# Kernel tuning notes

Measured on AMD Instinct MI355X. Metric: run time of the kernel, lower is better.

Reference implementation:

```python
import jax, jax.numpy as jnp
import numpy as np

N_NODES = 16384
N_EDGES = 262144
D = 256
B = 32            # graphs per batch; nodes_per_graph = N_NODES // B
N_LAYERS = 3
N_HIDDEN = 2


def setup_inputs() -> dict:
    key = jax.random.key(0)
    ks = jax.random.split(key, 10)
    s = 1.0 / np.sqrt(D)
    x = jax.random.normal(ks[0], (N_NODES, D), dtype=jnp.float32)
    edge_index = jax.random.randint(ks[1], (2, N_EDGES), 0, N_NODES, dtype=jnp.int64)
    # SAGEConv params: lin_l (applied to aggregated neighbors, has bias), lin_r (root, no bias)
    Wl = jax.random.uniform(ks[2], (N_LAYERS, D, D), jnp.float32, -s, s)
    bl = jax.random.uniform(ks[3], (N_LAYERS, D), jnp.float32, -s, s)
    Wr = jax.random.uniform(ks[4], (N_LAYERS, D, D), jnp.float32, -s, s)
    # post MLP: two relu hidden layers + linear output (rlkit Mlp defaults)
    Wh = jax.random.uniform(ks[5], (N_HIDDEN, D, D), jnp.float32, -s, s)
    bh = jax.random.uniform(ks[6], (N_HIDDEN, D), jnp.float32, -s, s)
    Wo = jax.random.uniform(ks[7], (D, D), jnp.float32, -s, s)
    bo = jax.random.uniform(ks[8], (D,), jnp.float32, -s, s)
    return {"x": x, "edge_index": edge_index, "Wl": Wl, "bl": bl, "Wr": Wr,
            "Wh": Wh, "bh": bh, "Wo": Wo, "bo": bo}


def reference(x, edge_index, Wl, bl, Wr, Wh, bh, Wo, bo):
    src, dst = edge_index[0], edge_index[1]
    # in-degree for mean aggregation (computed once; edge structure is fixed)
    deg = jax.ops.segment_sum(jnp.ones((src.shape[0],), x.dtype), dst,
                              num_segments=N_NODES)
    inv_deg = (1.0 / jnp.maximum(deg, 1.0))[:, None]          # [N,1]
    for l in range(N_LAYERS):
        # gather -> segment mean -> dual GEMM (SAGEConv, aggr='mean')
        agg = jax.ops.segment_sum(x[src], dst, num_segments=N_NODES) * inv_deg
        x = agg @ Wl[l] + bl[l] + x @ Wr[l]                   # [N,D]
    h = x.reshape(B, -1, D)[:, 0, :]                          # root node per graph [B,D]
    for l in range(N_HIDDEN):
        h = jax.nn.relu(h @ Wh[l] + bh[l])
    return h @ Wo + bo                                        # [B,D]
```

## Files before the change

### kernel.cpp

```cpp
#include <hip/hip_runtime.h>

#define N_NODES 16384
#define N_EDGES 262144
#define D 256
#define B_GRAPHS 32
#define NODES_PER_GRAPH 512
#define MAXDEG 64

__global__ __launch_bounds__(256) void zero_cnt_kernel(int* __restrict__ cnt) {
    cnt[blockIdx.x * 256 + threadIdx.x] = 0;
}

__global__ __launch_bounds__(256) void fill_bucket_kernel(const int* __restrict__ edge,
                                                          int* __restrict__ cnt,
                                                          int* __restrict__ col) {
    int e = blockIdx.x * 256 + threadIdx.x;
    int dst = edge[N_EDGES + e];
    int src = edge[e];
    int slot = atomicAdd(&cnt[dst], 1);
    if (slot < MAXDEG) col[dst * MAXDEG + slot] = src;
}

__global__ __launch_bounds__(256) void aggx_kernel(const float* __restrict__ x,
                                                   const int* __restrict__ cnt,
                                                   const int* __restrict__ col,
                                                   float* __restrict__ A) {
    int node = blockIdx.x * 4 + (threadIdx.x >> 6);
    int lane = threadIdx.x & 63;
    int c = cnt[node];
    if (c > MAXDEG) c = MAXDEG;
    int my = (lane < c) ? col[node * MAXDEG + lane] : 0;
    float a0 = 0.f, a1 = 0.f, a2 = 0.f, a3 = 0.f;
    int j = 0;
    for (; j + 8 <= c; j += 8) {
        float4 v[8];
        #pragma unroll
        for (int q = 0; q < 8; ++q) {
            int s = __shfl(my, j + q);
            v[q] = *(const float4*)&x[(size_t)s * D + lane * 4];
        }
        #pragma unroll
        for (int q = 0; q < 8; ++q) {
            a0 += v[q].x; a1 += v[q].y; a2 += v[q].z; a3 += v[q].w;
        }
    }
    for (; j < c; ++j) {
        int s = __shfl(my, j);
        float4 v = *(const float4*)&x[(size_t)s * D + lane * 4];
        a0 += v.x; a1 += v.y; a2 += v.z; a3 += v.w;
    }
    float id = 1.0f / (float)(c < 1 ? 1 : c);
    float4 r = make_float4(a0 * id, a1 * id, a2 * id, a3 * id);
    *(float4*)&A[(size_t)node * D + lane * 4] = r;
}

__global__ __launch_bounds__(1024) void tail_kernel(
    const int* __restrict__ cnt, const int* __restrict__ col,
    const float* __restrict__ x, const float* __restrict__ A,
    const float* __restrict__ Wl, const float* __restrict__ bl,
    const float* __restrict__ Wr,
    const float* __restrict__ Wh, const float* __restrict__ bh,
    const float* __restrict__ Wo, const float* __restrict__ bo,
    float* __restrict__ out)
{
    __shared__ float g0[D], g1[D], g2[D], g3[D];
    __shared__ float v0[D], v1[D], v2[D], hA[D], hB[D];
    __shared__ float part1[16][D];
    __shared__ float part2[16][D];
    __shared__ int nbr[MAXDEG];
    __shared__ int snr;

    const int b = blockIdx.x, t = threadIdx.x;
    const int w = t >> 6, lane = t & 63;
    const int root = b * NODES_PER_GRAPH;

    if (t == 0) { int cc = cnt[root]; snr = (cc > MAXDEG) ? MAXDEG : cc; }
    __syncthreads();
    const int c0 = snr;
    if (t < c0) nbr[t] = col[root * MAXDEG + t];
    if (t < D) {
        g0[t] = x[(size_t)root * D + t];
        g1[t] = A[(size_t)root * D + t];
    }
    __syncthreads();

    float p1[4] = {0.f, 0.f, 0.f, 0.f}, p2[4] = {0.f, 0.f, 0.f, 0.f};
    for (int i = w; i < c0; i += 16) {
        int n = nbr[i];
        {
            float4 v = *(const float4*)&A[(size_t)n * D + lane * 4];
            p1[0] += v.x; p1[1] += v.y; p1[2] += v.z; p1[3] += v.w;
        }
        int c = cnt[n]; if (c > MAXDEG) c = MAXDEG;
        int my = (lane < c) ? col[n * MAXDEG + lane] : 0;
        float a[4] = {0.f, 0.f, 0.f, 0.f};
        int j = 0;
        for (; j + 4 <= c; j += 4) {
            float4 v[4];
            #pragma unroll
            for (int q = 0; q < 4; ++q) {
                int s = __shfl(my, j + q);
                v[q] = *(const float4*)&A[(size_t)s * D + lane * 4];
            }
            #pragma unroll
            for (int q = 0; q < 4; ++q) {
                a[0] += v[q].x; a[1] += v[q].y; a[2] += v[q].z; a[3] += v[q].w;
            }
        }
        for (; j < c; ++j) {
            int s = __shfl(my, j);
            float4 v = *(const float4*)&A[(size_t)s * D + lane * 4];
            a[0] += v.x; a[1] += v.y; a[2] += v.z; a[3] += v.w;
        }
        float id = 1.0f / (float)(c < 1 ? 1 : c);
        #pragma unroll
        for (int q = 0; q < 4; ++q) p2[q] += a[q] * id;
    }
    #pragma unroll
    for (int q = 0; q < 4; ++q) {
        part1[w][lane * 4 + q] = p1[q];
        part2[w][lane * 4 + q] = p2[q];
    }
    __syncthreads();
    if (t < D) {
        float s1 = 0.f, s2 = 0.f;
        #pragma unroll
        for (int ww = 0; ww < 16; ++ww) { s1 += part1[ww][t]; s2 += part2[ww][t]; }
        float id0 = 1.0f / (float)(c0 < 1 ? 1 : c0);
        g2[t] = s1 * id0;
        g3[t] = s2 * id0;
    }
    __syncthreads();

    const int c = t & 255, kq = t >> 8;
    {
        const float* WL = Wl;
        const float* WR = Wr;
        float a0 = 0.f, a1 = 0.f, a2 = 0.f;
        #pragma unroll 8
        for (int k0 = 0; k0 < 64; ++k0) {
            int k = kq * 64 + k0;
            float wl = WL[(size_t)k * D + c];
            float wr = WR[(size_t)k * D + c];
            a0 += g1[k] * wl + g0[k] * wr;
            a1 += g2[k] * wl + g1[k] * wr;
            a2 += g3[k] * wl + g2[k] * wr;
        }
        part1[kq][c] = a0; part1[4 + kq][c] = a1; part1[8 + kq][c] = a2;
        __syncthreads();
        if (t < D) {
            float bb = bl[t];
            v0[t] = part1[0][t] + part1[1][t] + part1[2][t] + part1[3][t] + bb;
            v1[t] = part1[4][t] + part1[5][t] + part1[6][t] + part1[7][t] + bb;
            v2[t] = part1[8][t] + part1[9][t] + part1[10][t] + part1[11][t] + bb;
        }
        __syncthreads();
    }
    {
        const float* WL = Wl + (size_t)1 * D * D;
        const float* WR = Wr + (size_t)1 * D * D;
        float aA = 0.f, aB = 0.f;
        #pragma unroll 8
        for (int k0 = 0; k0 < 64; ++k0) {
            int k = kq * 64 + k0;
            float wl = WL[(size_t)k * D + c];
            float wr = WR[(size_t)k * D + c];
            aA += v2[k] * wl + v1[k] * wr;
            aB += v1[k] * wl + v0[k] * wr;
        }
        part1[kq][c] = aA; part1[4 + kq][c] = aB;
        __syncthreads();
        if (t < D) {
            float bb = bl[D + t];
            hA[t] = part1[0][t] + part1[1][t] + part1[2][t] + part1[3][t] + bb;
            hB[t] = part1[4][t] + part1[5][t] + part1[6][t] + part1[7][t] + bb;
        }
        __syncthreads();
    }
    {
        const float* WL = Wl + (size_t)2 * D * D;
        const float* WR = Wr + (size_t)2 * D * D;
        float acc = 0.f;
        #pragma unroll 8
        for (int k0 = 0; k0 < 64; ++k0) {
            int k = kq * 64 + k0;
            acc += hA[k] * WL[(size_t)k * D + c] + hB[k] * WR[(size_t)k * D + c];
        }
        part1[kq][c] = acc;
        __syncthreads();
        if (t < D) v0[t] = part1[0][t] + part1[1][t] + part1[2][t] + part1[3][t]
                           + bl[2 * D + t];
        __syncthreads();
    }
    for (int l = 0; l < 3; ++l) {
        const float* W = (l < 2) ? Wh + (size_t)l * D * D : Wo;
        float acc = 0.f;
        #pragma unroll 8
        for (int k0 = 0; k0 < 64; ++k0) {
            int k = kq * 64 + k0;
            acc += v0[k] * W[(size_t)k * D + c];
        }
        part1[kq][c] = acc;
        __syncthreads();
        if (t < D) {
            float v = part1[0][t] + part1[1][t] + part1[2][t] + part1[3][t]
                    + ((l < 2) ? bh[(size_t)l * D + t] : bo[t]);
            if (l < 2) v0[t] = fmaxf(v, 0.f);
            else       out[(size_t)b * D + t] = v;
        }
        __syncthreads();
    }
}

extern "C" void kernel_launch(void* const* d_in, const int* in_sizes, int n_in,
                              void* d_out, int out_size, void* d_ws, size_t ws_size,
                              hipStream_t stream) {
    const float* x    = (const float*)d_in[0];
    const int*   edge = (const int*)d_in[1];
    const float* Wl   = (const float*)d_in[2];
    const float* bl   = (const float*)d_in[3];
    const float* Wr   = (const float*)d_in[4];
    const float* Wh   = (const float*)d_in[5];
    const float* bh   = (const float*)d_in[6];
    const float* Wo   = (const float*)d_in[7];
    const float* bo   = (const float*)d_in[8];
    float* out = (float*)d_out;

    char* w = (char*)d_ws;
    auto alloc = [&](size_t bytes) {
        char* p = w;
        w += (bytes + 255) & ~(size_t)255;
        return p;
    };
    int*   cnt = (int*)  alloc((size_t)N_NODES * 4);
    int*   col = (int*)  alloc((size_t)N_NODES * MAXDEG * 4);
    float* A   = (float*)alloc((size_t)N_NODES * D * 4);

    zero_cnt_kernel<<<N_NODES / 256, 256, 0, stream>>>(cnt);
    fill_bucket_kernel<<<N_EDGES / 256, 256, 0, stream>>>(edge, cnt, col);
    aggx_kernel<<<N_NODES / 4, 256, 0, stream>>>(x, cnt, col, A);
    tail_kernel<<<B_GRAPHS, 1024, 0, stream>>>(cnt, col, x, A,
                                               Wl, bl, Wr, Wh, bh, Wo, bo, out);
}
```

Baseline: 94.94 us.

## Split root 2-hop neighbor aggregation into separate wide kernel, vectorize tail GEMVs

The second-hop neighbor aggregation for each graph's root now runs in a new kernel with one wavefront per (graph, neighbor slot), 2048 wavefronts in total. Before, it ran inside the 32-block tail kernel, so only 32 blocks did that work. The tail kernel now just sums the precomputed rows. Its GEMV loops also switch to float4 weight loads with 16 k-partitions instead of 4. The cost is one extra launch and a small workspace buffer.

```diff
diff --git a/kernel.cpp b/kernel.cpp
--- a/kernel.cpp
+++ b/kernel.cpp
@@ -54,9 +54,48 @@
     *(float4*)&A[(size_t)node * D + lane * 4] = r;
 }
 
+__global__ __launch_bounds__(256) void aggB_kernel(const float* __restrict__ A,
+                                                   const int* __restrict__ cnt,
+                                                   const int* __restrict__ col,
+                                                   float* __restrict__ B) {
+    int wg = blockIdx.x * 4 + (threadIdx.x >> 6);
+    int r = wg >> 6;
+    int slot = wg & 63;
+    int lane = threadIdx.x & 63;
+    int root = r * NODES_PER_GRAPH;
+    int c0 = cnt[root]; if (c0 > MAXDEG) c0 = MAXDEG;
+    if (slot >= c0) return;
+    int n = col[root * MAXDEG + slot];
+    int c = cnt[n]; if (c > MAXDEG) c = MAXDEG;
+    int my = (lane < c) ? col[n * MAXDEG + lane] : 0;
+    float a0 = 0.f, a1 = 0.f, a2 = 0.f, a3 = 0.f;
+    int j = 0;
+    for (; j + 8 <= c; j += 8) {
+        float4 v[8];
+        #pragma unroll
+        for (int q = 0; q < 8; ++q) {
+            int s = __shfl(my, j + q);
+            v[q] = *(const float4*)&A[(size_t)s * D + lane * 4];
+        }
+        #pragma unroll
+        for (int q = 0; q < 8; ++q) {
+            a0 += v[q].x; a1 += v[q].y; a2 += v[q].z; a3 += v[q].w;
+        }
+    }
+    for (; j < c; ++j) {
+        int s = __shfl(my, j);
+        float4 v = *(const float4*)&A[(size_t)s * D + lane * 4];
+        a0 += v.x; a1 += v.y; a2 += v.z; a3 += v.w;
+    }
+    float id = 1.0f / (float)(c < 1 ? 1 : c);
+    float4 out = make_float4(a0 * id, a1 * id, a2 * id, a3 * id);
+    *(float4*)&B[(size_t)wg * D + lane * 4] = out;
+}
+
 __global__ __launch_bounds__(1024) void tail_kernel(
     const int* __restrict__ cnt, const int* __restrict__ col,
     const float* __restrict__ x, const float* __restrict__ A,
+    const float* __restrict__ B,
     const float* __restrict__ Wl, const float* __restrict__ bl,
     const float* __restrict__ Wr,
     const float* __restrict__ Wh, const float* __restrict__ bh,
@@ -65,9 +104,7 @@
 {
     __shared__ float g0[D], g1[D], g2[D], g3[D];
     __shared__ float v0[D], v1[D], v2[D], hA[D], hB[D];
-    __shared__ float part1[16][D];
-    __shared__ float part2[16][D];
-    __shared__ int nbr[MAXDEG];
+    __shared__ float part[3][16][D];
     __shared__ int snr;
 
     const int b = blockIdx.x, t = threadIdx.x;
@@ -75,136 +112,139 @@
     const int root = b * NODES_PER_GRAPH;
 
     if (t == 0) { int cc = cnt[root]; snr = (cc > MAXDEG) ? MAXDEG : cc; }
-    __syncthreads();
-    const int c0 = snr;
-    if (t < c0) nbr[t] = col[root * MAXDEG + t];
     if (t < D) {
         g0[t] = x[(size_t)root * D + t];
         g1[t] = A[(size_t)root * D + t];
     }
     __syncthreads();
-
-    float p1[4] = {0.f, 0.f, 0.f, 0.f}, p2[4] = {0.f, 0.f, 0.f, 0.f};
-    for (int i = w; i < c0; i += 16) {
-        int n = nbr[i];
-        {
-            float4 v = *(const float4*)&A[(size_t)n * D + lane * 4];
-            p1[0] += v.x; p1[1] += v.y; p1[2] += v.z; p1[3] += v.w;
-        }
-        int c = cnt[n]; if (c > MAXDEG) c = MAXDEG;
-        int my = (lane < c) ? col[n * MAXDEG + lane] : 0;
-        float a[4] = {0.f, 0.f, 0.f, 0.f};
-        int j = 0;
-        for (; j + 4 <= c; j += 4) {
-            float4 v[4];
-            #pragma unroll
-            for (int q = 0; q < 4; ++q) {
-                int s = __shfl(my, j + q);
-                v[q] = *(const float4*)&A[(size_t)s * D + lane * 4];
+    const int c0 = snr;
+
+    {
+        float p1[4] = {0.f, 0.f, 0.f, 0.f}, p2[4] = {0.f, 0.f, 0.f, 0.f};
+        for (int i = w; i < c0; i += 16) {
+            int n = col[root * MAXDEG + i];
+            float4 va = *(const float4*)&A[(size_t)n * D + lane * 4];
+            float4 vb = *(const float4*)&B[(size_t)(b * MAXDEG + i) * D + lane * 4];
+            p1[0] += va.x; p1[1] += va.y; p1[2] += va.z; p1[3] += va.w;
+            p2[0] += vb.x; p2[1] += vb.y; p2[2] += vb.z; p2[3] += vb.w;
+        }
+        #pragma unroll
+        for (int q = 0; q < 4; ++q) {
+            part[0][w][lane * 4 + q] = p1[q];
+            part[1][w][lane * 4 + q] = p2[q];
+        }
+        __syncthreads();
+        if (t < D) {
+            float s1 = 0.f, s2 = 0.f;
+            #pragma unroll
+            for (int ww = 0; ww < 16; ++ww) { s1 += part[0][ww][t]; s2 += part[1][ww][t]; }
+            float id0 = 1.0f / (float)(c0 < 1 ? 1 : c0);
+            g2[t] = s1 * id0;
+            g3[t] = s2 * id0;
+        }
+        __syncthreads();
+    }
+
+    const int kq = t >> 6, c4 = t & 63;
+    {
+        const float4* WL = (const float4*)Wl;
+        const float4* WR = (const float4*)Wr;
+        float4 a0 = {0,0,0,0}, a1 = {0,0,0,0}, a2 = {0,0,0,0};
+        #pragma unroll
+        for (int k0 = 0; k0 < 16; ++k0) {
+            int k = kq * 16 + k0;
+            float4 wl = WL[(size_t)k * 64 + c4];
+            float4 wr = WR[(size_t)k * 64 + c4];
+            float h1 = g1[k], h0 = g0[k], h2 = g2[k], h3 = g3[k];
+            a0.x += h1 * wl.x + h0 * wr.x; a0.y += h1 * wl.y + h0 * wr.y;
+            a0.z += h1 * wl.z + h0 * wr.z; a0.w += h1 * wl.w + h0 * wr.w;
+            a1.x += h2 * wl.x + h1 * wr.x; a1.y += h2 * wl.y + h1 * wr.y;
+            a1.z += h2 * wl.z + h1 * wr.z; a1.w += h2 * wl.w + h1 * wr.w;
+            a2.x += h3 * wl.x + h2 * wr.x; a2.y += h3 * wl.y + h2 * wr.y;
+            a2.z += h3 * wl.z + h2 * wr.z; a2.w += h3 * wl.w + h2 * wr.w;
+        }
+        *(float4*)&part[0][kq][c4 * 4] = a0;
+        *(float4*)&part[1][kq][c4 * 4] = a1;
+        *(float4*)&part[2][kq][c4 * 4] = a2;
+        __syncthreads();
+        if (t < D) {
+            float s0 = 0.f, s1 = 0.f, s2 = 0.f;
+            #pragma unroll
+            for (int i = 0; i < 16; ++i) {
+                s0 += part[0][i][t]; s1 += part[1][i][t]; s2 += part[2][i][t];
             }
-            #pragma unroll
-            for (int q = 0; q < 4; ++q) {
-                a[0] += v[q].x; a[1] += v[q].y; a[2] += v[q].z; a[3] += v[q].w;
-            }
-        }
-        for (; j < c; ++j) {
-            int s = __shfl(my, j);
-            float4 v = *(const float4*)&A[(size_t)s * D + lane * 4];
-            a[0] += v.x; a[1] += v.y; a[2] += v.z; a[3] += v.w;
-        }
-        float id = 1.0f / (float)(c < 1 ? 1 : c);
-        #pragma unroll
-        for (int q = 0; q < 4; ++q) p2[q] += a[q] * id;
-    }
-    #pragma unroll
-    for (int q = 0; q < 4; ++q) {
-        part1[w][lane * 4 + q] = p1[q];
-        part2[w][lane * 4 + q] = p2[q];
-    }
-    __syncthreads();
-    if (t < D) {
-        float s1 = 0.f, s2 = 0.f;
-        #pragma unroll
-        for (int ww = 0; ww < 16; ++ww) { s1 += part1[ww][t]; s2 += part2[ww][t]; }
-        float id0 = 1.0f / (float)(c0 < 1 ? 1 : c0);
-        g2[t] = s1 * id0;
-        g3[t] = s2 * id0;
-    }
-    __syncthreads();
-
-    const int c = t & 255, kq = t >> 8;
-    {
-        const float* WL = Wl;
-        const float* WR = Wr;
-        float a0 = 0.f, a1 = 0.f, a2 = 0.f;
-        #pragma unroll 8
-        for (int k0 = 0; k0 < 64; ++k0) {
-            int k = kq * 64 + k0;
-            float wl = WL[(size_t)k * D + c];
-            float wr = WR[(size_t)k * D + c];
-            a0 += g1[k] * wl + g0[k] * wr;
-            a1 += g2[k] * wl + g1[k] * wr;
-            a2 += g3[k] * wl + g2[k] * wr;
-        }
-        part1[kq][c] = a0; part1[4 + kq][c] = a1; part1[8 + kq][c] = a2;
-        __syncthreads();
-        if (t < D) {
             float bb = bl[t];
-            v0[t] = part1[0][t] + part1[1][t] + part1[2][t] + part1[3][t] + bb;
-            v1[t] = part1[4][t] + part1[5][t] + part1[6][t] + part1[7][t] + bb;
-            v2[t] = part1[8][t] + part1[9][t] + part1[10][t] + part1[11][t] + bb;
-        }
-        __syncthreads();
-    }
-    {
-        const float* WL = Wl + (size_t)1 * D * D;
-        const float* WR = Wr + (size_t)1 * D * D;
-        float aA = 0.f, aB = 0.f;
-        #pragma unroll 8
-        for (int k0 = 0; k0 < 64; ++k0) {
-            int k = kq * 64 + k0;
-            float wl = WL[(size_t)k * D + c];
-            float wr = WR[(size_t)k * D + c];
-            aA += v2[k] * wl + v1[k] * wr;
-            aB += v1[k] * wl + v0[k] * wr;
-        }
-        part1[kq][c] = aA; part1[4 + kq][c] = aB;
-        __syncthreads();
-        if (t < D) {
+            v0[t] = s0 + bb; v1[t] = s1 + bb; v2[t] = s2 + bb;
+        }
+        __syncthreads();
+    }
+    {
+        const float4* WL = (const float4*)(Wl + (size_t)1 * D * D);
+        const float4* WR = (const float4*)(Wr + (size_t)1 * D * D);
+        float4 aA = {0,0,0,0}, aB = {0,0,0,0};
+        #pragma unroll
+        for (int k0 = 0; k0 < 16; ++k0) {
+            int k = kq * 16 + k0;
+            float4 wl = WL[(size_t)k * 64 + c4];
+            float4 wr = WR[(size_t)k * 64 + c4];
+            float h2 = v2[k], h1 = v1[k], h0 = v0[k];
+            aA.x += h2 * wl.x + h1 * wr.x; aA.y += h2 * wl.y + h1 * wr.y;
+            aA.z += h2 * wl.z + h1 * wr.z; aA.w += h2 * wl.w + h1 * wr.w;
+            aB.x += h1 * wl.x + h0 * wr.x; aB.y += h1 * wl.y + h0 * wr.y;
+            aB.z += h1 * wl.z + h0 * wr.z; aB.w += h1 * wl.w + h0 * wr.w;
+        }
+        *(float4*)&part[0][kq][c4 * 4] = aA;
+        *(float4*)&part[1][kq][c4 * 4] = aB;
+        __syncthreads();
+        if (t < D) {
+            float sA = 0.f, sB = 0.f;
+            #pragma unroll
+            for (int i = 0; i < 16; ++i) { sA += part[0][i][t]; sB += part[1][i][t]; }
             float bb = bl[D + t];
-            hA[t] = part1[0][t] + part1[1][t] + part1[2][t] + part1[3][t] + bb;
-            hB[t] = part1[4][t] + part1[5][t] + part1[6][t] + part1[7][t] + bb;
-        }
-        __syncthreads();
-    }
-    {
-        const float* WL = Wl + (size_t)2 * D * D;
-        const float* WR = Wr + (size_t)2 * D * D;
-        float acc = 0.f;
-        #pragma unroll 8
-        for (int k0 = 0; k0 < 64; ++k0) {
-            int k = kq * 64 + k0;
-            acc += hA[k] * WL[(size_t)k * D + c] + hB[k] * WR[(size_t)k * D + c];
-        }
-        part1[kq][c] = acc;
-        __syncthreads();
-        if (t < D) v0[t] = part1[0][t] + part1[1][t] + part1[2][t] + part1[3][t]
-                           + bl[2 * D + t];
+            hA[t] = sA + bb; hB[t] = sB + bb;
+        }
+        __syncthreads();
+    }
+    {
+        const float4* WL = (const float4*)(Wl + (size_t)2 * D * D);
+        const float4* WR = (const float4*)(Wr + (size_t)2 * D * D);
+        float4 a = {0,0,0,0};
+        #pragma unroll
+        for (int k0 = 0; k0 < 16; ++k0) {
+            int k = kq * 16 + k0;
+            float4 wl = WL[(size_t)k * 64 + c4];
+            float4 wr = WR[(size_t)k * 64 + c4];
+            float ha = hA[k], hb = hB[k];
+            a.x += ha * wl.x + hb * wr.x; a.y += ha * wl.y + hb * wr.y;
+            a.z += ha * wl.z + hb * wr.z; a.w += ha * wl.w + hb * wr.w;
+        }
+        *(float4*)&part[0][kq][c4 * 4] = a;
+        __syncthreads();
+        if (t < D) {
+            float s = 0.f;
+            #pragma unroll
+            for (int i = 0; i < 16; ++i) s += part[0][i][t];
+            v0[t] = s + bl[2 * D + t];
+        }
         __syncthreads();
     }
     for (int l = 0; l < 3; ++l) {
-        const float* W = (l < 2) ? Wh + (size_t)l * D * D : Wo;
-        float acc = 0.f;
-        #pragma unroll 8
-        for (int k0 = 0; k0 < 64; ++k0) {
-            int k = kq * 64 + k0;
-            acc += v0[k] * W[(size_t)k * D + c];
-        }
-        part1[kq][c] = acc;
-        __syncthreads();
-        if (t < D) {
-            float v = part1[0][t] + part1[1][t] + part1[2][t] + part1[3][t]
-                    + ((l < 2) ? bh[(size_t)l * D + t] : bo[t]);
+        const float4* W = (const float4*)((l < 2) ? Wh + (size_t)l * D * D : Wo);
+        float4 a = {0,0,0,0};
+        #pragma unroll
+        for (int k0 = 0; k0 < 16; ++k0) {
+            int k = kq * 16 + k0;
+            float4 wv = W[(size_t)k * 64 + c4];
+            float hk = v0[k];
+            a.x += hk * wv.x; a.y += hk * wv.y; a.z += hk * wv.z; a.w += hk * wv.w;
+        }
+        *(float4*)&part[0][kq][c4 * 4] = a;
+        __syncthreads();
+        if (t < D) {
+            float s = 0.f;
+            #pragma unroll
+            for (int i = 0; i < 16; ++i) s += part[0][i][t];
+            float v = s + ((l < 2) ? bh[(size_t)l * D + t] : bo[t]);
             if (l < 2) v0[t] = fmaxf(v, 0.f);
             else       out[(size_t)b * D + t] = v;
         }
@@ -235,10 +275,12 @@
     int*   cnt = (int*)  alloc((size_t)N_NODES * 4);
     int*   col = (int*)  alloc((size_t)N_NODES * MAXDEG * 4);
     float* A   = (float*)alloc((size_t)N_NODES * D * 4);
+    float* B   = (float*)alloc((size_t)B_GRAPHS * MAXDEG * D * 4);
 
     zero_cnt_kernel<<<N_NODES / 256, 256, 0, stream>>>(cnt);
     fill_bucket_kernel<<<N_EDGES / 256, 256, 0, stream>>>(edge, cnt, col);
     aggx_kernel<<<N_NODES / 4, 256, 0, stream>>>(x, cnt, col, A);
-    tail_kernel<<<B_GRAPHS, 1024, 0, stream>>>(cnt, col, x, A,
+    aggB_kernel<<<512, 256, 0, stream>>>(A, cnt, col, B);
+    tail_kernel<<<B_GRAPHS, 1024, 0, stream>>>(cnt, col, x, A, B,
                                                Wl, bl, Wr, Wh, bh, Wo, bo, out);
 }
```

New measurement: 113.0 us, median of 2. 19.0% more time.

## Prefetch weights into L2 during aggregation and batch weight loads in tail

Applied to the files above, without the earlier changes.

Adds 36 extra blocks to the aggregation kernel that read all Wl, Wr, Wh and Wo weights into cache, so the single-wave tail kernel finds them warm in L2 instead of fetching them cold from HBM. The tail kernel's GEMV loops now load 16 or 32 weight values into registers before the FMAs, giving more loads in flight. The neighbor-of-neighbor gather unroll goes from 4 to 8. The cost is extra register pressure in the 1024-thread tail kernel and a small amount of wasted bandwidth during aggregation.

```diff
diff --git a/kernel.cpp b/kernel.cpp
--- a/kernel.cpp
+++ b/kernel.cpp
@@ -6,6 +6,7 @@
 #define B_GRAPHS 32
 #define NODES_PER_GRAPH 512
 #define MAXDEG 64
+#define NWARM 36
 
 __global__ __launch_bounds__(256) void zero_cnt_kernel(int* __restrict__ cnt) {
     cnt[blockIdx.x * 256 + threadIdx.x] = 0;
@@ -24,9 +25,33 @@
 __global__ __launch_bounds__(256) void aggx_kernel(const float* __restrict__ x,
                                                    const int* __restrict__ cnt,
                                                    const int* __restrict__ col,
-                                                   float* __restrict__ A) {
-    int node = blockIdx.x * 4 + (threadIdx.x >> 6);
-    int lane = threadIdx.x & 63;
+                                                   float* __restrict__ A,
+                                                   const float* __restrict__ Wl,
+                                                   const float* __restrict__ Wr,
+                                                   const float* __restrict__ Wh,
+                                                   const float* __restrict__ Wo,
+                                                   float* __restrict__ warm) {
+    const int bid = blockIdx.x;
+    const int t = threadIdx.x;
+    if (bid >= 4096) {
+        int wb = bid - 4096;
+        float s = 0.f;
+        #pragma unroll
+        for (int i = 0; i < 16; ++i) {
+            size_t fidx = ((size_t)wb * 4096 + i * 256 + t) * 4;
+            const float* src; size_t off = fidx;
+            if (off < 196608)      { src = Wl; }
+            else if (off < 393216) { src = Wr; off -= 196608; }
+            else if (off < 524288) { src = Wh; off -= 393216; }
+            else                   { src = Wo; off -= 524288; }
+            float4 v = *(const float4*)&src[off];
+            s += v.x + v.y + v.z + v.w;
+        }
+        warm[wb * 256 + t] = s;
+        return;
+    }
+    int node = bid * 4 + (t >> 6);
+    int lane = t & 63;
     int c = cnt[node];
     if (c > MAXDEG) c = MAXDEG;
     int my = (lane < c) ? col[node * MAXDEG + lane] : 0;
@@ -84,75 +109,88 @@
     }
     __syncthreads();
 
-    float p1[4] = {0.f, 0.f, 0.f, 0.f}, p2[4] = {0.f, 0.f, 0.f, 0.f};
-    for (int i = w; i < c0; i += 16) {
-        int n = nbr[i];
-        {
-            float4 v = *(const float4*)&A[(size_t)n * D + lane * 4];
-            p1[0] += v.x; p1[1] += v.y; p1[2] += v.z; p1[3] += v.w;
-        }
-        int c = cnt[n]; if (c > MAXDEG) c = MAXDEG;
-        int my = (lane < c) ? col[n * MAXDEG + lane] : 0;
-        float a[4] = {0.f, 0.f, 0.f, 0.f};
-        int j = 0;
-        for (; j + 4 <= c; j += 4) {
-            float4 v[4];
-            #pragma unroll
-            for (int q = 0; q < 4; ++q) {
-                int s = __shfl(my, j + q);
-                v[q] = *(const float4*)&A[(size_t)s * D + lane * 4];
-            }
-            #pragma unroll
-            for (int q = 0; q < 4; ++q) {
-                a[0] += v[q].x; a[1] += v[q].y; a[2] += v[q].z; a[3] += v[q].w;
-            }
-        }
-        for (; j < c; ++j) {
-            int s = __shfl(my, j);
-            float4 v = *(const float4*)&A[(size_t)s * D + lane * 4];
-            a[0] += v.x; a[1] += v.y; a[2] += v.z; a[3] += v.w;
-        }
-        float id = 1.0f / (float)(c < 1 ? 1 : c);
+    {
+        float p1[4] = {0.f, 0.f, 0.f, 0.f}, p2[4] = {0.f, 0.f, 0.f, 0.f};
+        for (int i = w; i < c0; i += 16) {
+            int n = nbr[i];
+            {
+                float4 v = *(const float4*)&A[(size_t)n * D + lane * 4];
+                p1[0] += v.x; p1[1] += v.y; p1[2] += v.z; p1[3] += v.w;
+            }
+            int c = cnt[n]; if (c > MAXDEG) c = MAXDEG;
+            int my = (lane < c) ? col[n * MAXDEG + lane] : 0;
+            float a[4] = {0.f, 0.f, 0.f, 0.f};
+            int j = 0;
+            for (; j + 8 <= c; j += 8) {
+                float4 v[8];
+                #pragma unroll
+                for (int q = 0; q < 8; ++q) {
+                    int s = __shfl(my, j + q);
+                    v[q] = *(const float4*)&A[(size_t)s * D + lane * 4];
+                }
+                #pragma unroll
+                for (int q = 0; q < 8; ++q) {
+                    a[0] += v[q].x; a[1] += v[q].y; a[2] += v[q].z; a[3] += v[q].w;
+                }
+            }
+            for (; j < c; ++j) {
+                int s = __shfl(my, j);
+                float4 v = *(const float4*)&A[(size_t)s * D + lane * 4];
+                a[0] += v.x; a[1] += v.y; a[2] += v.z; a[3] += v.w;
+            }
+            float id = 1.0f / (float)(c < 1 ? 1 : c);
+            #pragma unroll
+            for (int q = 0; q < 4; ++q) p2[q] += a[q] * id;
+        }
         #pragma unroll
-        for (int q = 0; q < 4; ++q) p2[q] += a[q] * id;
-    }
-    #pragma unroll
-    for (int q = 0; q < 4; ++q) {
-        part1[w][lane * 4 + q] = p1[q];
-        part2[w][lane * 4 + q] = p2[q];
-    }
-    __syncthreads();
-    if (t < D) {
-        float s1 = 0.f, s2 = 0.f;
-        #pragma unroll
-        for (int ww = 0; ww < 16; ++ww) { s1 += part1[ww][t]; s2 += part2[ww][t]; }
-        float id0 = 1.0f / (float)(c0 < 1 ? 1 : c0);
-        g2[t] = s1 * id0;
-        g3[t] = s2 * id0;
-    }
-    __syncthreads();
+        for (int q = 0; q < 4; ++q) {
+            part1[w][lane * 4 + q] = p1[q];
+            part2[w][lane * 4 + q] = p2[q];
+        }
+        __syncthreads();
+        if (t < D) {
+            float s1 = 0.f, s2 = 0.f;
+            #pragma unroll
+            for (int ww = 0; ww < 16; ++ww) { s1 += part1[ww][t]; s2 += part2[ww][t]; }
+            float id0 = 1.0f / (float)(c0 < 1 ? 1 : c0);
+            g2[t] = s1 * id0;
+            g3[t] = s2 * id0;
+        }
+        __syncthreads();
+    }
 
     const int c = t & 255, kq = t >> 8;
     {
         const float* WL = Wl;
         const float* WR = Wr;
         float a0 = 0.f, a1 = 0.f, a2 = 0.f;
-        #pragma unroll 8
-        for (int k0 = 0; k0 < 64; ++k0) {
-            int k = kq * 64 + k0;
-            float wl = WL[(size_t)k * D + c];
-            float wr = WR[(size_t)k * D + c];
-            a0 += g1[k] * wl + g0[k] * wr;
-            a1 += g2[k] * wl + g1[k] * wr;
-            a2 += g3[k] * wl + g2[k] * wr;
+        for (int kb = 0; kb < 64; kb += 16) {
+            float wl[16], wr[16];
+            #pragma unroll
+            for (int q = 0; q < 16; ++q) {
+                int k = kq * 64 + kb + q;
+                wl[q] = WL[(size_t)k * D + c];
+                wr[q] = WR[(size_t)k * D + c];
+            }
+            #pragma unroll
+            for (int q = 0; q < 16; ++q) {
+                int k = kq * 64 + kb + q;
+                float h0 = g0[k], h1 = g1[k], h2 = g2[k], h3 = g3[k];
+                a0 += h1 * wl[q] + h0 * wr[q];
+                a1 += h2 * wl[q] + h1 * wr[q];
+                a2 += h3 * wl[q] + h2 * wr[q];
+            }
         }
         part1[kq][c] = a0; part1[4 + kq][c] = a1; part1[8 + kq][c] = a2;
         __syncthreads();
         if (t < D) {
+            float s0 = 0.f, s1 = 0.f, s2 = 0.f;
+            #pragma unroll
+            for (int i = 0; i < 4; ++i) {
+                s0 += part1[i][t]; s1 += part1[4 + i][t]; s2 += part1[8 + i][t];
+            }
             float bb = bl[t];
-            v0[t] = part1[0][t] + part1[1][t] + part1[2][t] + part1[3][t] + bb;
-            v1[t] = part1[4][t] + part1[5][t] + part1[6][t] + part1[7][t] + bb;
-            v2[t] = part1[8][t] + part1[9][t] + part1[10][t] + part1[11][t] + bb;
+            v0[t] = s0 + bb; v1[t] = s1 + bb; v2[t] = s2 + bb;
         }
         __syncthreads();
     }
@@ -160,51 +198,80 @@
         const float* WL = Wl + (size_t)1 * D * D;
         const float* WR = Wr + (size_t)1 * D * D;
         float aA = 0.f, aB = 0.f;
-        #pragma unroll 8
-        for (int k0 = 0; k0 < 64; ++k0) {
-            int k = kq * 64 + k0;
-            float wl = WL[(size_t)k * D + c];
-            float wr = WR[(size_t)k * D + c];
-            aA += v2[k] * wl + v1[k] * wr;
-            aB += v1[k] * wl + v0[k] * wr;
+        for (int kb = 0; kb < 64; kb += 16) {
+            float wl[16], wr[16];
+            #pragma unroll
+            for (int q = 0; q < 16; ++q) {
+                int k = kq * 64 + kb + q;
+                wl[q] = WL[(size_t)k * D + c];
+                wr[q] = WR[(size_t)k * D + c];
+            }
+            #pragma unroll
+            for (int q = 0; q < 16; ++q) {
+                int k = kq * 64 + kb + q;
+                float h2 = v2[k], h1 = v1[k], h0 = v0[k];
+                aA += h2 * wl[q] + h1 * wr[q];
+                aB += h1 * wl[q] + h0 * wr[q];
+            }
         }
         part1[kq][c] = aA; part1[4 + kq][c] = aB;
         __syncthreads();
         if (t < D) {
+            float sA = 0.f, sB = 0.f;
+            #pragma unroll
+            for (int i = 0; i < 4; ++i) { sA += part1[i][t]; sB += part1[4 + i][t]; }
             float bb = bl[D + t];
-            hA[t] = part1[0][t] + part1[1][t] + part1[2][t] + part1[3][t] + bb;
-            hB[t] = part1[4][t] + part1[5][t] + part1[6][t] + part1[7][t] + bb;
+            hA[t] = sA + bb; hB[t] = sB + bb;
         }
         __syncthreads();
     }
     {
         const float* WL = Wl + (size_t)2 * D * D;
         const float* WR = Wr + (size_t)2 * D * D;
-        float acc = 0.f;
-        #pragma unroll 8
-        for (int k0 = 0; k0 < 64; ++k0) {
-            int k = kq * 64 + k0;
-            acc += hA[k] * WL[(size_t)k * D + c] + hB[k] * WR[(size_t)k * D + c];
-        }
-        part1[kq][c] = acc;
-        __syncthreads();
-        if (t < D) v0[t] = part1[0][t] + part1[1][t] + part1[2][t] + part1[3][t]
-                           + bl[2 * D + t];
+        float a = 0.f;
+        for (int kb = 0; kb < 64; kb += 16) {
+            float wl[16], wr[16];
+            #pragma unroll
+            for (int q = 0; q < 16; ++q) {
+                int k = kq * 64 + kb + q;
+                wl[q] = WL[(size_t)k * D + c];
+                wr[q] = WR[(size_t)k * D + c];
+            }
+            #pragma unroll
+            for (int q = 0; q < 16; ++q) {
+                int k = kq * 64 + kb + q;
+                a += hA[k] * wl[q] + hB[k] * wr[q];
+            }
+        }
+        part1[kq][c] = a;
+        __syncthreads();
+        if (t < D) {
+            float s = 0.f;
+            #pragma unroll
+            for (int i = 0; i < 4; ++i) s += part1[i][t];
+            v0[t] = s + bl[2 * D + t];
+        }
         __syncthreads();
     }
     for (int l = 0; l < 3; ++l) {
         const float* W = (l < 2) ? Wh + (size_t)l * D * D : Wo;
-        float acc = 0.f;
-        #pragma unroll 8
-        for (int k0 = 0; k0 < 64; ++k0) {
-            int k = kq * 64 + k0;
-            acc += v0[k] * W[(size_t)k * D + c];
-        }
-        part1[kq][c] = acc;
-        __syncthreads();
-        if (t < D) {
-            float v = part1[0][t] + part1[1][t] + part1[2][t] + part1[3][t]
-                    + ((l < 2) ? bh[(size_t)l * D + t] : bo[t]);
+        float a = 0.f;
+        for (int kb = 0; kb < 64; kb += 32) {
+            float wv[32];
+            #pragma unroll
+            for (int q = 0; q < 32; ++q)
+                wv[q] = W[(size_t)(kq * 64 + kb + q) * D + c];
+            #pragma unroll
+            for (int q = 0; q < 32; ++q)
+                a += v0[kq * 64 + kb + q] * wv[q];
+        }
+        part1[kq][c] = a;
+        __syncthreads();
+        if (t < D) {
+            float s = 0.f;
+            #pragma unroll
+            for (int i = 0; i < 4; ++i) s += part1[i][t];
+            float v = s + ((l < 2) ? bh[(size_t)l * D + t] : bo[t]);
             if (l < 2) v0[t] = fmaxf(v, 0.f);
             else       out[(size_t)b * D + t] = v;
         }
@@ -232,13 +299,15 @@
         w += (bytes + 255) & ~(size_t)255;
         return p;
     };
-    int*   cnt = (int*)  alloc((size_t)N_NODES * 4);
-    int*   col = (int*)  alloc((size_t)N_NODES * MAXDEG * 4);
-    float* A   = (float*)alloc((size_t)N_NODES * D * 4);
+    int*   cnt  = (int*)  alloc((size_t)N_NODES * 4);
+    int*   col  = (int*)  alloc((size_t)N_NODES * MAXDEG * 4);
+    float* A    = (float*)alloc((size_t)N_NODES * D * 4);
+    float* warm = (float*)alloc((size_t)NWARM * 256 * 4);
 
     zero_cnt_kernel<<<N_NODES / 256, 256, 0, stream>>>(cnt);
     fill_bucket_kernel<<<N_EDGES / 256, 256, 0, stream>>>(edge, cnt, col);
-    aggx_kernel<<<N_NODES / 4, 256, 0, stream>>>(x, cnt, col, A);
+    aggx_kernel<<<4096 + NWARM, 256, 0, stream>>>(x, cnt, col, A,
+                                                  Wl, Wr, Wh, Wo, warm);
     tail_kernel<<<B_GRAPHS, 1024, 0, stream>>>(cnt, col, x, A,
                                                Wl, bl, Wr, Wh, bh, Wo, bo, out);
 }
```

Result: slower. 133.4 us (+40.5%).

## Precompose SAGE layer weight products into Q matrices computed alongside edge/aggregation kernels

Applied to the files above, without the earlier changes.

Because the SAGE layers are linear, the three layers' Wl/Wr matrices are pre-multiplied into four composite 256x256 matrices Q (plus an effective bias), so the tail needs one four-term matvec instead of three dependent layered GEMV stages. The weight products run as extra blocks inside the edge-bucketing and aggregation kernels, overlapping the scatter/gather work. This trades serial per-graph tail work for redundant dense GEMM work per call and changes floating-point association. The tail's neighbor gather is also unrolled by eight, and the MLP loads are batched.

```diff
diff --git a/kernel.cpp b/kernel.cpp
--- a/kernel.cpp
+++ b/kernel.cpp
@@ -11,60 +11,179 @@
     cnt[blockIdx.x * 256 + threadIdx.x] = 0;
 }
 
-__global__ __launch_bounds__(256) void fill_bucket_kernel(const int* __restrict__ edge,
-                                                          int* __restrict__ cnt,
-                                                          int* __restrict__ col) {
-    int e = blockIdx.x * 256 + threadIdx.x;
-    int dst = edge[N_EDGES + e];
-    int src = edge[e];
-    int slot = atomicAdd(&cnt[dst], 1);
-    if (slot < MAXDEG) col[dst * MAXDEG + slot] = src;
-}
-
-__global__ __launch_bounds__(256) void aggx_kernel(const float* __restrict__ x,
-                                                   const int* __restrict__ cnt,
-                                                   const int* __restrict__ col,
-                                                   float* __restrict__ A) {
-    int node = blockIdx.x * 4 + (threadIdx.x >> 6);
-    int lane = threadIdx.x & 63;
-    int c = cnt[node];
-    if (c > MAXDEG) c = MAXDEG;
-    int my = (lane < c) ? col[node * MAXDEG + lane] : 0;
-    float a0 = 0.f, a1 = 0.f, a2 = 0.f, a3 = 0.f;
-    int j = 0;
-    for (; j + 8 <= c; j += 8) {
-        float4 v[8];
-        #pragma unroll
-        for (int q = 0; q < 8; ++q) {
-            int s = __shfl(my, j + q);
-            v[q] = *(const float4*)&x[(size_t)s * D + lane * 4];
-        }
-        #pragma unroll
-        for (int q = 0; q < 8; ++q) {
-            a0 += v[q].x; a1 += v[q].y; a2 += v[q].z; a3 += v[q].w;
-        }
-    }
-    for (; j < c; ++j) {
-        int s = __shfl(my, j);
-        float4 v = *(const float4*)&x[(size_t)s * D + lane * 4];
-        a0 += v.x; a1 += v.y; a2 += v.z; a3 += v.w;
-    }
-    float id = 1.0f / (float)(c < 1 ? 1 : c);
-    float4 r = make_float4(a0 * id, a1 * id, a2 * id, a3 * id);
-    *(float4*)&A[(size_t)node * D + lane * 4] = r;
+__device__ __forceinline__ void mm_tile32(const float* __restrict__ A,
+                                          const float* __restrict__ B,
+                                          int r0, int c0,
+                                          float (*As)[257], float acc[4]) {
+    const int t = threadIdx.x;
+    __syncthreads();
+    #pragma unroll
+    for (int i = 0; i < 8; ++i) {
+        int idx = i * 256 + t;
+        int r = idx >> 6, cq = idx & 63;
+        float4 v = *(const float4*)&A[(size_t)(r0 + r) * D + cq * 4];
+        As[r][cq * 4 + 0] = v.x; As[r][cq * 4 + 1] = v.y;
+        As[r][cq * 4 + 2] = v.z; As[r][cq * 4 + 3] = v.w;
+    }
+    __syncthreads();
+    const int c = c0 + (t & 31);
+    const int rb = t >> 5;
+    #pragma unroll 8
+    for (int k = 0; k < 256; ++k) {
+        float bv = B[(size_t)k * D + c];
+        acc[0] += As[rb][k] * bv;
+        acc[1] += As[rb + 8][k] * bv;
+        acc[2] += As[rb + 16][k] * bv;
+        acc[3] += As[rb + 24][k] * bv;
+    }
+}
+
+__device__ __forceinline__ void mm_store(float* __restrict__ O, int r0, int c0,
+                                         const float acc[4]) {
+    const int t = threadIdx.x;
+    const int c = c0 + (t & 31);
+    const int rb = t >> 5;
+    #pragma unroll
+    for (int q = 0; q < 4; ++q)
+        O[(size_t)(r0 + rb + q * 8) * D + c] = acc[q];
+}
+
+__global__ __launch_bounds__(256) void fill_p_kernel(
+    const int* __restrict__ edge, int* __restrict__ cnt, int* __restrict__ col,
+    const float* __restrict__ Wl, const float* __restrict__ Wr,
+    const float* __restrict__ bl,
+    float* __restrict__ P2, float* __restrict__ P1, float* __restrict__ P0,
+    float* __restrict__ bias2)
+{
+    __shared__ float As[32][257];
+    const int bid = blockIdx.x;
+    const int t = threadIdx.x;
+    if (bid < 1024) {
+        int e = bid * 256 + t;
+        int dst = edge[N_EDGES + e];
+        int src = edge[e];
+        int slot = atomicAdd(&cnt[dst], 1);
+        if (slot < MAXDEG) col[dst * MAXDEG + slot] = src;
+        return;
+    }
+    if (bid == 1216) {
+        const float* b2 = bl + D;
+        const float* b3 = bl + 2 * D;
+        const float* L3 = Wl + (size_t)2 * D * D;
+        const float* R3 = Wr + (size_t)2 * D * D;
+        float s = 0.f;
+        #pragma unroll 8
+        for (int k = 0; k < D; ++k)
+            s += b2[k] * (L3[(size_t)k * D + t] + R3[(size_t)k * D + t]);
+        bias2[t] = s + b3[t];
+        return;
+    }
+    int pb = bid - 1024;
+    int mat = pb >> 6, tile = pb & 63;
+    int r0 = (tile >> 3) * 32, c0 = (tile & 7) * 32;
+    const float* L2 = Wl + (size_t)1 * D * D;
+    const float* R2 = Wr + (size_t)1 * D * D;
+    const float* L3 = Wl + (size_t)2 * D * D;
+    const float* R3 = Wr + (size_t)2 * D * D;
+    float acc[4] = {0.f, 0.f, 0.f, 0.f};
+    if (mat == 0) {
+        mm_tile32(L2, L3, r0, c0, As, acc);
+        mm_store(P2, r0, c0, acc);
+    } else if (mat == 1) {
+        mm_tile32(R2, L3, r0, c0, As, acc);
+        mm_tile32(L2, R3, r0, c0, As, acc);
+        mm_store(P1, r0, c0, acc);
+    } else {
+        mm_tile32(R2, R3, r0, c0, As, acc);
+        mm_store(P0, r0, c0, acc);
+    }
+}
+
+__global__ __launch_bounds__(256) void aggx_q_kernel(
+    const float* __restrict__ x, const int* __restrict__ cnt,
+    const int* __restrict__ col, float* __restrict__ A,
+    const float* __restrict__ Wl, const float* __restrict__ Wr,
+    const float* __restrict__ bl,
+    const float* __restrict__ P2, const float* __restrict__ P1,
+    const float* __restrict__ P0, const float* __restrict__ bias2,
+    float* __restrict__ Q, float* __restrict__ beff)
+{
+    __shared__ float As[32][257];
+    const int bid = blockIdx.x;
+    const int t = threadIdx.x;
+    if (bid < 4096) {
+        int node = bid * 4 + (t >> 6);
+        int lane = t & 63;
+        int c = cnt[node];
+        if (c > MAXDEG) c = MAXDEG;
+        int my = (lane < c) ? col[node * MAXDEG + lane] : 0;
+        float a0 = 0.f, a1 = 0.f, a2 = 0.f, a3 = 0.f;
+        int j = 0;
+        for (; j + 8 <= c; j += 8) {
+            float4 v[8];
+            #pragma unroll
+            for (int q = 0; q < 8; ++q) {
+                int s = __shfl(my, j + q);
+                v[q] = *(const float4*)&x[(size_t)s * D + lane * 4];
+            }
+            #pragma unroll
+            for (int q = 0; q < 8; ++q) {
+                a0 += v[q].x; a1 += v[q].y; a2 += v[q].z; a3 += v[q].w;
+            }
+        }
+        for (; j < c; ++j) {
+            int s = __shfl(my, j);
+            float4 v = *(const float4*)&x[(size_t)s * D + lane * 4];
+            a0 += v.x; a1 += v.y; a2 += v.z; a3 += v.w;
+        }
+        float id = 1.0f / (float)(c < 1 ? 1 : c);
+        float4 r = make_float4(a0 * id, a1 * id, a2 * id, a3 * id);
+        *(float4*)&A[(size_t)node * D + lane * 4] = r;
+        return;
+    }
+    if (bid == 4352) {
+        const float* b1 = bl;
+        float s = 0.f;
+        #pragma unroll 8
+        for (int k = 0; k < D; ++k)
+            s += b1[k] * (P2[(size_t)k * D + t] + P1[(size_t)k * D + t]
+                        + P0[(size_t)k * D + t]);
+        beff[t] = s + bias2[t];
+        return;
+    }
+    int qb = bid - 4096;
+    int mat = qb >> 6, tile = qb & 63;
+    int r0 = (tile >> 3) * 32, c0 = (tile & 7) * 32;
+    const float* L1 = Wl;
+    const float* R1 = Wr;
+    float acc[4] = {0.f, 0.f, 0.f, 0.f};
+    if (mat == 0) {
+        mm_tile32(L1, P2, r0, c0, As, acc);
+        mm_store(Q + 3 * (size_t)D * D, r0, c0, acc);
+    } else if (mat == 1) {
+        mm_tile32(R1, P2, r0, c0, As, acc);
+        mm_tile32(L1, P1, r0, c0, As, acc);
+        mm_store(Q + 2 * (size_t)D * D, r0, c0, acc);
+    } else if (mat == 2) {
+        mm_tile32(R1, P1, r0, c0, As, acc);
+        mm_tile32(L1, P0, r0, c0, As, acc);
+        mm_store(Q + 1 * (size_t)D * D, r0, c0, acc);
+    } else {
+        mm_tile32(R1, P0, r0, c0, As, acc);
+        mm_store(Q + 0 * (size_t)D * D, r0, c0, acc);
+    }
 }
 
 __global__ __launch_bounds__(1024) void tail_kernel(
     const int* __restrict__ cnt, const int* __restrict__ col,
     const float* __restrict__ x, const float* __restrict__ A,
-    const float* __restrict__ Wl, const float* __restrict__ bl,
-    const float* __restrict__ Wr,
+    const float* __restrict__ Q, const float* __restrict__ beff,
     const float* __restrict__ Wh, const float* __restrict__ bh,
     const float* __restrict__ Wo, const float* __restrict__ bo,
     float* __restrict__ out)
 {
     __shared__ float g0[D], g1[D], g2[D], g3[D];
-    __shared__ float v0[D], v1[D], v2[D], hA[D], hB[D];
+    __shared__ float v0[D];
     __shared__ float part1[16][D];
     __shared__ float part2[16][D];
     __shared__ int nbr[MAXDEG];
@@ -84,123 +203,91 @@
     }
     __syncthreads();
 
-    float p1[4] = {0.f, 0.f, 0.f, 0.f}, p2[4] = {0.f, 0.f, 0.f, 0.f};
-    for (int i = w; i < c0; i += 16) {
-        int n = nbr[i];
-        {
-            float4 v = *(const float4*)&A[(size_t)n * D + lane * 4];
-            p1[0] += v.x; p1[1] += v.y; p1[2] += v.z; p1[3] += v.w;
-        }
-        int c = cnt[n]; if (c > MAXDEG) c = MAXDEG;
-        int my = (lane < c) ? col[n * MAXDEG + lane] : 0;
-        float a[4] = {0.f, 0.f, 0.f, 0.f};
-        int j = 0;
-        for (; j + 4 <= c; j += 4) {
-            float4 v[4];
-            #pragma unroll
-            for (int q = 0; q < 4; ++q) {
-                int s = __shfl(my, j + q);
-                v[q] = *(const float4*)&A[(size_t)s * D + lane * 4];
-            }
-            #pragma unroll
-            for (int q = 0; q < 4; ++q) {
-                a[0] += v[q].x; a[1] += v[q].y; a[2] += v[q].z; a[3] += v[q].w;
-            }
-        }
-        for (; j < c; ++j) {
-            int s = __shfl(my, j);
-            float4 v = *(const float4*)&A[(size_t)s * D + lane * 4];
-            a[0] += v.x; a[1] += v.y; a[2] += v.z; a[3] += v.w;
-        }
-        float id = 1.0f / (float)(c < 1 ? 1 : c);
+    {
+        float p1[4] = {0.f, 0.f, 0.f, 0.f}, p2[4] = {0.f, 0.f, 0.f, 0.f};
+        for (int i = w; i < c0; i += 16) {
+            int n = nbr[i];
+            {
+                float4 v = *(const float4*)&A[(size_t)n * D + lane * 4];
+                p1[0] += v.x; p1[1] += v.y; p1[2] += v.z; p1[3] += v.w;
+            }
+            int c = cnt[n]; if (c > MAXDEG) c = MAXDEG;
+            int my = (lane < c) ? col[n * MAXDEG + lane] : 0;
+            float a[4] = {0.f, 0.f, 0.f, 0.f};
+            int j = 0;
+            for (; j + 8 <= c; j += 8) {
+                float4 v[8];
+                #pragma unroll
+                for (int q = 0; q < 8; ++q) {
+                    int s = __shfl(my, j + q);
+                    v[q] = *(const float4*)&A[(size_t)s * D + lane * 4];
+                }
+                #pragma unroll
+                for (int q = 0; q < 8; ++q) {
+                    a[0] += v[q].x; a[1] += v[q].y; a[2] += v[q].z; a[3] += v[q].w;
+                }
+            }
+            for (; j < c; ++j) {
+                int s = __shfl(my, j);
+                float4 v = *(const float4*)&A[(size_t)s * D + lane * 4];
+                a[0] += v.x; a[1] += v.y; a[2] += v.z; a[3] += v.w;
+            }
+            float id = 1.0f / (float)(c < 1 ? 1 : c);
+            #pragma unroll
+            for (int q = 0; q < 4; ++q) p2[q] += a[q] * id;
+        }
         #pragma unroll
-        for (int q = 0; q < 4; ++q) p2[q] += a[q] * id;
-    }
-    #pragma unroll
-    for (int q = 0; q < 4; ++q) {
-        part1[w][lane * 4 + q] = p1[q];
-        part2[w][lane * 4 + q] = p2[q];
-    }
-    __syncthreads();
-    if (t < D) {
-        float s1 = 0.f, s2 = 0.f;
-        #pragma unroll
-        for (int ww = 0; ww < 16; ++ww) { s1 += part1[ww][t]; s2 += part2[ww][t]; }
-        float id0 = 1.0f / (float)(c0 < 1 ? 1 : c0);
-        g2[t] = s1 * id0;
-        g3[t] = s2 * id0;
-    }
-    __syncthreads();
+        for (int q = 0; q < 4; ++q) {
+            part1[w][lane * 4 + q] = p1[q];
+            part2[w][lane * 4 + q] = p2[q];
+        }
+        __syncthreads();
+        if (t < D) {
+            float s1 = 0.f, s2 = 0.f;
+            #pragma unroll
+            for (int ww = 0; ww < 16; ++ww) { s1 += part1[ww][t]; s2 += part2[ww][t]; }
+            float id0 = 1.0f / (float)(c0 < 1 ? 1 : c0);
+            g2[t] = s1 * id0;
+            g3[t] = s2 * id0;
+        }
+        __syncthreads();
+    }
 
     const int c = t & 255, kq = t >> 8;
     {
-        const float* WL = Wl;
-        const float* WR = Wr;
-        float a0 = 0.f, a1 = 0.f, a2 = 0.f;
+        const float* Q0 = Q;
+        const float* Q1 = Q + (size_t)D * D;
+        const float* Q2 = Q + 2 * (size_t)D * D;
+        const float* Q3 = Q + 3 * (size_t)D * D;
+        float a = 0.f;
         #pragma unroll 8
         for (int k0 = 0; k0 < 64; ++k0) {
             int k = kq * 64 + k0;
-            float wl = WL[(size_t)k * D + c];
-            float wr = WR[(size_t)k * D + c];
-            a0 += g1[k] * wl + g0[k] * wr;
-            a1 += g2[k] * wl + g1[k] * wr;
-            a2 += g3[k] * wl + g2[k] * wr;
-        }
-        part1[kq][c] = a0; part1[4 + kq][c] = a1; part1[8 + kq][c] = a2;
+            a += g0[k] * Q0[(size_t)k * D + c] + g1[k] * Q1[(size_t)k * D + c]
+               + g2[k] * Q2[(size_t)k * D + c] + g3[k] * Q3[(size_t)k * D + c];
+        }
+        part1[kq][c] = a;
         __syncthreads();
         if (t < D) {
-            float bb = bl[t];
-            v0[t] = part1[0][t] + part1[1][t] + part1[2][t] + part1[3][t] + bb;
-            v1[t] = part1[4][t] + part1[5][t] + part1[6][t] + part1[7][t] + bb;
-            v2[t] = part1[8][t] + part1[9][t] + part1[10][t] + part1[11][t] + bb;
-        }
-        __syncthreads();
-    }
-    {
-        const float* WL = Wl + (size_t)1 * D * D;
-        const float* WR = Wr + (size_t)1 * D * D;
-        float aA = 0.f, aB = 0.f;
-        #pragma unroll 8
-        for (int k0 = 0; k0 < 64; ++k0) {
-            int k = kq * 64 + k0;
-            float wl = WL[(size_t)k * D + c];
-            float wr = WR[(size_t)k * D + c];
-            aA += v2[k] * wl + v1[k] * wr;
-            aB += v1[k] * wl + v0[k] * wr;
-        }
-        part1[kq][c] = aA; part1[4 + kq][c] = aB;
-        __syncthreads();
-        if (t < D) {
-            float bb = bl[D + t];
-            hA[t] = part1[0][t] + part1[1][t] + part1[2][t] + part1[3][t] + bb;
-            hB[t] = part1[4][t] + part1[5][t] + part1[6][t] + part1[7][t] + bb;
-        }
-        __syncthreads();
-    }
-    {
-        const float* WL = Wl + (size_t)2 * D * D;
-        const float* WR = Wr + (size_t)2 * D * D;
-        float acc = 0.f;
-        #pragma unroll 8
-        for (int k0 = 0; k0 < 64; ++k0) {
-            int k = kq * 64 + k0;
-            acc += hA[k] * WL[(size_t)k * D + c] + hB[k] * WR[(size_t)k * D + c];
-        }
-        part1[kq][c] = acc;
-        __syncthreads();
-        if (t < D) v0[t] = part1[0][t] + part1[1][t] + part1[2][t] + part1[3][t]
-                           + bl[2 * D + t];
+            float s = part1[0][t] + part1[1][t] + part1[2][t] + part1[3][t];
+            v0[t] = s + beff[t];
+        }
         __syncthreads();
     }
     for (int l = 0; l < 3; ++l) {
         const float* W = (l < 2) ? Wh + (size_t)l * D * D : Wo;
-        float acc = 0.f;
-        #pragma unroll 8
-        for (int k0 = 0; k0 < 64; ++k0) {
-            int k = kq * 64 + k0;
-            acc += v0[k] * W[(size_t)k * D + c];
-        }
-        part1[kq][c] = acc;
+        float a = 0.f;
+        #pragma unroll
+        for (int k0 = 0; k0 < 64; k0 += 8) {
+            float wv[8];
+            #pragma unroll
+            for (int j = 0; j < 8; ++j)
+                wv[j] = W[(size_t)(kq * 64 + k0 + j) * D + c];
+            #pragma unroll
+            for (int j = 0; j < 8; ++j)
+                a += v0[kq * 64 + k0 + j] * wv[j];
+        }
+        part1[kq][c] = a;
         __syncthreads();
         if (t < D) {
             float v = part1[0][t] + part1[1][t] + part1[2][t] + part1[3][t]
@@ -232,13 +319,21 @@
         w += (bytes + 255) & ~(size_t)255;
         return p;
     };
-    int*   cnt = (int*)  alloc((size_t)N_NODES * 4);
-    int*   col = (int*)  alloc((size_t)N_NODES * MAXDEG * 4);
-    float* A   = (float*)alloc((size_t)N_NODES * D * 4);
+    int*   cnt   = (int*)  alloc((size_t)N_NODES * 4);
+    int*   col   = (int*)  alloc((size_t)N_NODES * MAXDEG * 4);
+    float* A     = (float*)alloc((size_t)N_NODES * D * 4);
+    float* P2    = (float*)alloc((size_t)D * D * 4);
+    float* P1    = (float*)alloc((size_t)D * D * 4);
+    float* P0    = (float*)alloc((size_t)D * D * 4);
+    float* bias2 = (float*)alloc((size_t)D * 4);
+    float* Q     = (float*)alloc((size_t)4 * D * D * 4);
+    float* beff  = (float*)alloc((size_t)D * 4);
 
     zero_cnt_kernel<<<N_NODES / 256, 256, 0, stream>>>(cnt);
-    fill_bucket_kernel<<<N_EDGES / 256, 256, 0, stream>>>(edge, cnt, col);
-    aggx_kernel<<<N_NODES / 4, 256, 0, stream>>>(x, cnt, col, A);
-    tail_kernel<<<B_GRAPHS, 1024, 0, stream>>>(cnt, col, x, A,
-                                               Wl, bl, Wr, Wh, bh, Wo, bo, out);
-}
+    fill_p_kernel<<<1217, 256, 0, stream>>>(edge, cnt, col, Wl, Wr, bl,
+                                            P2, P1, P0, bias2);
+    aggx_q_kernel<<<4353, 256, 0, stream>>>(x, cnt, col, A, Wl, Wr, bl,
+                                            P2, P1, P0, bias2, Q, beff);
+    tail_kernel<<<B_GRAPHS, 1024, 0, stream>>>(cnt, col, x, A, Q, beff,
+                                               Wh, bh, Wo, bo, out);
+}
```

Result: slower. 129.6 us (+36.5%).
